# Optimization experiments

Measured on AMD Instinct MI355X. Metric: run time of the kernel, lower is better.

## Reference

```python
import jax, jax.numpy as jnp
import numpy as np

NO_ENTITIES = 1_000_000
NO_RELATIONSHIPS = 1_000
DIM = 10
LAMBDA = 1.0
B, S = 16384, 128


def setup_inputs() -> dict:
    key = jax.random.key(0)
    k_e1, k_r, k_e2, k_ee, k_re, k_w, k_b = jax.random.split(key, 7)
    e1 = jax.random.randint(k_e1, (B, S), 0, NO_ENTITIES)
    rl = jax.random.randint(k_r, (B, S), 0, NO_RELATIONSHIPS)
    e2 = jax.random.randint(k_e2, (B, S), 0, NO_ENTITIES)
    samples = jnp.stack([e1, rl, e2], axis=-1)  # [B, S, 3] int
    ent_emb = jax.random.normal(k_ee, (NO_ENTITIES, DIM), dtype=jnp.float32)
    rel_emb = jax.random.normal(k_re, (NO_RELATIONSHIPS, DIM), dtype=jnp.float32)
    W = jax.random.uniform(k_w, (DIM, DIM), dtype=jnp.float32)
    b = jax.random.uniform(k_b, (DIM,), dtype=jnp.float32)
    return {"samples": samples, "ent_emb": ent_emb, "rel_emb": rel_emb, "W": W, "b": b}


def _circular_correl(e1, e2):
    # irfft(conj(rfft(e1)) * rfft(e2)) with onesided=False == real part of ifft(conj(fft(e1))*fft(e2))
    return jnp.fft.ifft(jnp.conj(jnp.fft.fft(e1, axis=-1)) * jnp.fft.fft(e2, axis=-1), axis=-1).real.astype(e1.dtype)


def reference(samples, ent_emb, rel_emb, W, b):
    lam = LAMBDA
    entity_1 = ent_emb[samples[:, :, 0]]   # [B,S,D]
    r = rel_emb[samples[:, :, 1]]          # [B,S,D]
    entity_2 = ent_emb[samples[:, :, 2]]   # [B,S,D]
    x = r * _circular_correl(entity_1, entity_2)  # harmonic holographic embedding [B,S,D]

    Wsym = W + W.T
    # muy: h = (-0.5*b + lam*x) @ (Wsym - lam*I)^{-1}
    V = jnp.linalg.inv(Wsym - lam * jnp.eye(DIM, dtype=W.dtype))
    h = jnp.einsum('bsk,kt->bst', -0.5 * b + lam * x, V)  # [B,S,D]

    # H(h, x): quadratic form + linear term - lam*||h-x||^2 -> [B,S]
    hW = jnp.einsum('bsj,jk->bsk', h, Wsym)
    quad = jnp.einsum('bsk,bsk->bs', hW, h)
    lin = jnp.einsum('bsk,k->bs', h, b)
    diff = h - x
    nrm = jnp.einsum('bsk,bsk->bs', diff, diff)
    return quad + lin - lam * nrm
```

## Files before the change

### kernel.cpp

```cpp
#include <hip/hip_runtime.h>
#include <math.h>

#define DIM 10

__global__ __launch_bounds__(128) void harmon_setup(const float* __restrict__ W,
                                                    const float* __restrict__ b,
                                                    float* __restrict__ ws) {
    __shared__ double Ws[DIM][DIM];
    __shared__ double Aug[DIM][2 * DIM];
    __shared__ double Vv[DIM][DIM];
    __shared__ double VW[DIM][DIM];
    __shared__ double M[DIM][DIM];
    __shared__ double colv[DIM];
    __shared__ double cvec[DIM], Vb[DIM], VTc[DIM];
    __shared__ int piv_s;

    const int t = threadIdx.x;

    for (int idx = t; idx < DIM * DIM; idx += 128) {
        int i = idx / DIM, j = idx % DIM;
        double w = (double)W[i * DIM + j] + (double)W[j * DIM + i];
        Ws[i][j] = w;
        Aug[i][j] = w - (i == j ? 1.0 : 0.0);
        Aug[i][DIM + j] = (i == j) ? 1.0 : 0.0;
    }
    if (t < DIM) cvec[t] = -0.5 * (double)b[t];
    __syncthreads();

    for (int col = 0; col < DIM; col++) {
        if (t == 0) {
            int piv = col;
            double best = fabs(Aug[col][col]);
            for (int r = col + 1; r < DIM; r++) {
                double v = fabs(Aug[r][col]);
                if (v > best) { best = v; piv = r; }
            }
            piv_s = piv;
        }
        __syncthreads();
        int piv = piv_s;
        if (piv != col && t < 2 * DIM) {
            double tmp = Aug[col][t]; Aug[col][t] = Aug[piv][t]; Aug[piv][t] = tmp;
        }
        __syncthreads();
        if (t < DIM) colv[t] = Aug[t][col];
        __syncthreads();
        if (t < 2 * DIM) Aug[col][t] /= colv[col];
        __syncthreads();
        for (int idx = t; idx < DIM * 2 * DIM; idx += 128) {
            int r = idx / (2 * DIM), j = idx % (2 * DIM);
            if (r != col) Aug[r][j] -= colv[r] * Aug[col][j];
        }
        __syncthreads();
    }

    for (int idx = t; idx < DIM * DIM; idx += 128) {
        int i = idx / DIM, j = idx % DIM;
        Vv[i][j] = Aug[i][DIM + j];
    }
    __syncthreads();

    for (int idx = t; idx < DIM * DIM; idx += 128) {
        int i = idx / DIM, k = idx % DIM;
        double s = 0;
        for (int j = 0; j < DIM; j++) s += Vv[i][j] * Ws[j][k];
        VW[i][k] = s;
    }
    __syncthreads();

    for (int idx = t; idx < DIM * DIM; idx += 128) {
        int i = idx / DIM, k = idx % DIM;
        double s = 0;
        for (int j = 0; j < DIM; j++) s += VW[i][j] * Vv[k][j];
        M[i][k] = s;
    }
    __syncthreads();

    for (int idx = t; idx < DIM * DIM; idx += 128) {
        int i = idx / DIM, k = idx % DIM;
        double s = 0;
        for (int j = 0; j < DIM; j++) {
            double ni = Vv[i][j] - (i == j ? 1.0 : 0.0);
            double nk = Vv[k][j] - (k == j ? 1.0 : 0.0);
            s += ni * nk;
        }
        ws[idx] = (float)(M[i][k] - s);
    }

    if (t < DIM) {
        double s = 0;
        for (int j = 0; j < DIM; j++) s += Vv[t][j] * (double)b[j];
        Vb[t] = s;
        double s2 = 0;
        for (int j = 0; j < DIM; j++) s2 += Vv[j][t] * cvec[j];
        VTc[t] = s2;
    }
    __syncthreads();

    if (t < DIM) {
        double s = 0;
        for (int j = 0; j < DIM; j++) {
            double nm = Vv[t][j] - (t == j ? 1.0 : 0.0);
            s += 2.0 * M[t][j] * cvec[j] - 2.0 * nm * VTc[j];
        }
        ws[100 + t] = (float)(s + Vb[t]);
    }
    __syncthreads();

    if (t == 0) {
        double cMc = 0, cVb = 0, n0 = 0;
        for (int i = 0; i < DIM; i++) {
            for (int j = 0; j < DIM; j++) cMc += cvec[i] * M[i][j] * cvec[j];
            cVb += cvec[i] * Vb[i];
            n0 += VTc[i] * VTc[i];
        }
        ws[110] = (float)(cMc + cVb - n0);
    }
}

__global__ __launch_bounds__(256) void harmon_main(
    const int* __restrict__ samples, const float* __restrict__ ent,
    const float* __restrict__ rel, const float* __restrict__ ws,
    float* __restrict__ out, int n) {
    int tid = blockIdx.x * 256 + threadIdx.x;
    if (tid >= n) return;

    int i1 = samples[3 * tid + 0];
    int ir = samples[3 * tid + 1];
    int i2 = samples[3 * tid + 2];

    const float2* p1 = (const float2*)(ent + (size_t)i1 * DIM);
    const float2* p2 = (const float2*)(ent + (size_t)i2 * DIM);
    const float2* pr = (const float2*)(rel + (size_t)ir * DIM);

    float a[DIM], e[DIM], r[DIM];
#pragma unroll
    for (int i = 0; i < 5; i++) {
        float2 v1 = p1[i]; a[2 * i] = v1.x; a[2 * i + 1] = v1.y;
        float2 v2 = p2[i]; e[2 * i] = v2.x; e[2 * i + 1] = v2.y;
        float2 vr = pr[i]; r[2 * i] = vr.x; r[2 * i + 1] = vr.y;
    }

    float x[DIM];
#pragma unroll
    for (int k = 0; k < DIM; k++) {
        float s = 0.0f;
#pragma unroll
        for (int j = 0; j < DIM; j++) s = fmaf(a[j], e[(j + k) % DIM], s);
        x[k] = r[k] * s;
    }

    float acc = ws[110];
#pragma unroll
    for (int k = 0; k < DIM; k++) {
        float s = ws[100 + k];
#pragma unroll
        for (int t = 0; t < DIM; t++) s = fmaf(ws[k * DIM + t], x[t], s);
        acc = fmaf(x[k], s, acc);
    }
    out[tid] = acc;
}

extern "C" void kernel_launch(void* const* d_in, const int* in_sizes, int n_in,
                              void* d_out, int out_size, void* d_ws, size_t ws_size,
                              hipStream_t stream) {
    const int* samples = (const int*)d_in[0];
    const float* ent = (const float*)d_in[1];
    const float* rel = (const float*)d_in[2];
    const float* W = (const float*)d_in[3];
    const float* b = (const float*)d_in[4];
    float* out = (float*)d_out;
    float* ws = (float*)d_ws;

    int n = in_sizes[0] / 3;

    harmon_setup<<<1, 128, 0, stream>>>(W, b, ws);
    int blocks = (n + 255) / 256;
    harmon_main<<<blocks, 256, 0, stream>>>(samples, ent, rel, ws, out, n);
}
```

Before: 101.1 us.

## Repack entity table to bf16 and gather from the compact copy

Adds a per-call kernel that converts the fp32 entity embedding table to bf16 in workspace, then gathers entity rows from the half-size table in the main kernel. Index loads and output stores become nontemporal. The goal is to halve the bytes moved by random row gathers, at the cost of a full streaming pass over the table each call and reduced precision of the embeddings. An fp32 fallback path is kept for when workspace is too small.

Result: no change. 99.37 us (-1.7%).

```diff
diff --git a/kernel.cpp b/kernel.cpp
--- a/kernel.cpp
+++ b/kernel.cpp
@@ -118,16 +118,88 @@
     }
 }
 
-__global__ __launch_bounds__(256) void harmon_main(
+__device__ __forceinline__ ushort f2bf_rne(float f) {
+    union { float f; unsigned u; } x; x.f = f;
+    unsigned u = x.u;
+    unsigned r = (u + 0x7FFFu + ((u >> 16) & 1u)) >> 16;
+    return (ushort)r;
+}
+
+__global__ __launch_bounds__(256) void repack_ent(const float* __restrict__ ent,
+                                                  ushort* __restrict__ tab, int n4) {
+    int i = blockIdx.x * 256 + threadIdx.x;
+    if (i >= n4) return;
+    float4 v = ((const float4*)ent)[i];
+    ushort4 o;
+    o.x = f2bf_rne(v.x);
+    o.y = f2bf_rne(v.y);
+    o.z = f2bf_rne(v.z);
+    o.w = f2bf_rne(v.w);
+    ((ushort4*)tab)[i] = o;
+}
+
+__device__ __forceinline__ float bf_lo(unsigned d) {
+    union { unsigned u; float f; } x; x.u = d << 16; return x.f;
+}
+__device__ __forceinline__ float bf_hi(unsigned d) {
+    union { unsigned u; float f; } x; x.u = d & 0xFFFF0000u; return x.f;
+}
+
+__global__ __launch_bounds__(256) void harmon_main_bf16(
+    const int* __restrict__ samples, const ushort* __restrict__ tab,
+    const float* __restrict__ rel, const float* __restrict__ ws,
+    float* __restrict__ out, int n) {
+    int tid = blockIdx.x * 256 + threadIdx.x;
+    if (tid >= n) return;
+
+    const int* sp = samples + 3 * (size_t)tid;
+    int i1 = __builtin_nontemporal_load(sp + 0);
+    int ir = __builtin_nontemporal_load(sp + 1);
+    int i2 = __builtin_nontemporal_load(sp + 2);
+
+    const unsigned* p1 = (const unsigned*)(tab + (size_t)i1 * DIM);
+    const unsigned* p2 = (const unsigned*)(tab + (size_t)i2 * DIM);
+    const float2* pr = (const float2*)(rel + (size_t)ir * DIM);
+
+    float a[DIM], e[DIM], r[DIM];
+#pragma unroll
+    for (int i = 0; i < 5; i++) {
+        unsigned d1 = p1[i]; a[2 * i] = bf_lo(d1); a[2 * i + 1] = bf_hi(d1);
+        unsigned d2 = p2[i]; e[2 * i] = bf_lo(d2); e[2 * i + 1] = bf_hi(d2);
+        float2 vr = pr[i]; r[2 * i] = vr.x; r[2 * i + 1] = vr.y;
+    }
+
+    float x[DIM];
+#pragma unroll
+    for (int k = 0; k < DIM; k++) {
+        float s = 0.0f;
+#pragma unroll
+        for (int j = 0; j < DIM; j++) s = fmaf(a[j], e[(j + k) % DIM], s);
+        x[k] = r[k] * s;
+    }
+
+    float acc = ws[110];
+#pragma unroll
+    for (int k = 0; k < DIM; k++) {
+        float s = ws[100 + k];
+#pragma unroll
+        for (int t = 0; t < DIM; t++) s = fmaf(ws[k * DIM + t], x[t], s);
+        acc = fmaf(x[k], s, acc);
+    }
+    __builtin_nontemporal_store(acc, out + tid);
+}
+
+__global__ __launch_bounds__(256) void harmon_main_f32(
     const int* __restrict__ samples, const float* __restrict__ ent,
     const float* __restrict__ rel, const float* __restrict__ ws,
     float* __restrict__ out, int n) {
     int tid = blockIdx.x * 256 + threadIdx.x;
     if (tid >= n) return;
 
-    int i1 = samples[3 * tid + 0];
-    int ir = samples[3 * tid + 1];
-    int i2 = samples[3 * tid + 2];
+    const int* sp = samples + 3 * (size_t)tid;
+    int i1 = __builtin_nontemporal_load(sp + 0);
+    int ir = __builtin_nontemporal_load(sp + 1);
+    int i2 = __builtin_nontemporal_load(sp + 2);
 
     const float2* p1 = (const float2*)(ent + (size_t)i1 * DIM);
     const float2* p2 = (const float2*)(ent + (size_t)i2 * DIM);
@@ -158,7 +230,7 @@
         for (int t = 0; t < DIM; t++) s = fmaf(ws[k * DIM + t], x[t], s);
         acc = fmaf(x[k], s, acc);
     }
-    out[tid] = acc;
+    __builtin_nontemporal_store(acc, out + tid);
 }
 
 extern "C" void kernel_launch(void* const* d_in, const int* in_sizes, int n_in,
@@ -173,8 +245,19 @@
     float* ws = (float*)d_ws;
 
     int n = in_sizes[0] / 3;
+    int ent_elems = in_sizes[1];
 
     harmon_setup<<<1, 128, 0, stream>>>(W, b, ws);
+
+    size_t need = 128 * sizeof(float) + (size_t)ent_elems * sizeof(ushort);
     int blocks = (n + 255) / 256;
-    harmon_main<<<blocks, 256, 0, stream>>>(samples, ent, rel, ws, out, n);
-}
+
+    if (ws_size >= need && (ent_elems & 3) == 0) {
+        ushort* tab = (ushort*)(ws + 128);
+        int n4 = ent_elems >> 2;
+        repack_ent<<<(n4 + 255) / 256, 256, 0, stream>>>(ent, tab, n4);
+        harmon_main_bf16<<<blocks, 256, 0, stream>>>(samples, tab, rel, ws, out, n);
+    } else {
+        harmon_main_f32<<<blocks, 256, 0, stream>>>(samples, ent, rel, ws, out, n);
+    }
+}
```
